# Optimization experiments

Hardware: AMD Instinct MI355X
Metric: run time of the kernel (lower is better)

Reference implementation:

```python
import math
import jax, jax.numpy as jnp
import numpy as np

D_MODEL, N_HEADS, D_FF = 2048, 16, 8192
B, T = 4, 1024
D_HEAD = D_MODEL // N_HEADS
LN_EPS = 1e-5


def hadamard(x):
    """Orthonormal Hadamard transform along last dim (power-of-two length)."""
    n = x.shape[-1]
    y = x.reshape(-1, n)
    h = 1
    while h < n:
        y = y.reshape(-1, n // (2 * h), 2, h)
        a, b = y[..., 0, :], y[..., 1, :]
        y = jnp.concatenate([a + b, a - b], axis=-1).reshape(-1, n)
        h *= 2
    return (y / math.sqrt(n)).reshape(x.shape)


def quantize_int8_per_row(W):
    s = jnp.maximum(jnp.max(jnp.abs(W), axis=1, keepdims=True), 1e-8) / 127.0
    Q = jnp.clip(jnp.round(W / s), -127, 127).astype(jnp.int8)
    return Q, s


def make_dtdr_weight(key, out_f, in_f):
    W = jax.random.normal(key, (out_f, in_f), dtype=jnp.float32) * 0.02
    return quantize_int8_per_row(hadamard(W))  # W_tilde = W @ H, then int8


def setup_inputs() -> dict:
    key = jax.random.key(0)
    ks = jax.random.split(key, 8)
    x = jax.random.normal(ks[0], (B, T, D_MODEL), dtype=jnp.float32)
    Qq, sq = make_dtdr_weight(ks[1], D_MODEL, D_MODEL)
    Qk, sk = make_dtdr_weight(ks[2], D_MODEL, D_MODEL)
    Qv, sv = make_dtdr_weight(ks[3], D_MODEL, D_MODEL)
    Qo, so = make_dtdr_weight(ks[4], D_MODEL, D_MODEL)
    Qf1, sf1 = make_dtdr_weight(ks[5], D_FF, D_MODEL)
    Qf2, sf2 = make_dtdr_weight(ks[6], D_MODEL, D_FF)
    return dict(
        x=x,
        ln1_g=jnp.ones((D_MODEL,), jnp.float32), ln1_b=jnp.zeros((D_MODEL,), jnp.float32),
        ln2_g=jnp.ones((D_MODEL,), jnp.float32), ln2_b=jnp.zeros((D_MODEL,), jnp.float32),
        Qq=Qq, sq=sq, Qk=Qk, sk=sk, Qv=Qv, sv=sv, Qo=Qo, so=so,
        Qf1=Qf1, sf1=sf1, bf1=jnp.zeros((D_FF,), jnp.float32),
        Qf2=Qf2, sf2=sf2, bf2=jnp.zeros((D_MODEL,), jnp.float32),
    )


def layernorm(x, g, b):
    mu = jnp.mean(x, axis=-1, keepdims=True)
    var = jnp.mean(jnp.square(x - mu), axis=-1, keepdims=True)
    return (x - mu) / jnp.sqrt(var + LN_EPS) * g + b


def dtdr_linear(x, Q, s, bias=None):
    # y = (H x) @ dequant(Q)^T + b
    xh = hadamard(x.astype(jnp.float32))
    W = Q.astype(jnp.float32) * s  # (out, in)
    y = jnp.einsum('btd,od->bto', xh, W)
    return y if bias is None else y + bias


def reference(x, ln1_g, ln1_b, ln2_g, ln2_b, Qq, sq, Qk, sk, Qv, sv, Qo, so,
              Qf1, sf1, bf1, Qf2, sf2, bf2):
    Bc, Tc, C = x.shape
    h = layernorm(x, ln1_g, ln1_b)
    q = dtdr_linear(h, Qq, sq).reshape(Bc, Tc, N_HEADS, D_HEAD).transpose(0, 2, 1, 3)
    k = dtdr_linear(h, Qk, sk).reshape(Bc, Tc, N_HEADS, D_HEAD).transpose(0, 2, 1, 3)
    v = dtdr_linear(h, Qv, sv).reshape(Bc, Tc, N_HEADS, D_HEAD).transpose(0, 2, 1, 3)
    scores = jnp.einsum('bhqd,bhkd->bhqk', q, k) / math.sqrt(D_HEAD)
    p = jax.nn.softmax(scores, axis=-1)
    out = jnp.einsum('bhqk,bhkd->bhqd', p, v)
    out = out.transpose(0, 2, 1, 3).reshape(Bc, Tc, C)
    x = x + dtdr_linear(out, Qo, so)
    h = layernorm(x, ln2_g, ln2_b)
    ff = dtdr_linear(h, Qf1, sf1, bf1)
    ff = jax.nn.gelu(ff, approximate=False)  # torch F.gelu default = erf gelu
    x = x + dtdr_linear(ff, Qf2, sf2, bf2)
    return x
```

## Files before the change

### kernel.cpp

```cpp
#include <hip/hip_runtime.h>
#include <cstdint>
#include <cstddef>

typedef unsigned short u16;
typedef unsigned int   u32;
typedef __bf16 bf16x8 __attribute__((ext_vector_type(8)));
typedef float  f32x4  __attribute__((ext_vector_type(4)));

__device__ __forceinline__ float bf2f(u16 u) {
  union { u32 i; float f; } v; v.i = ((u32)u) << 16; return v.f;
}
__device__ __forceinline__ u16 f2bf(float f) {
  union { float f; u32 i; } v; v.f = f;
  u32 r = v.i + 0x7fffu + ((v.i >> 16) & 1u);
  return (u16)(r >> 16);
}
__device__ __forceinline__ void unpack8(uint4 raw, float* v) {
  v[0]=bf2f(raw.x&0xffff); v[1]=bf2f(raw.x>>16);
  v[2]=bf2f(raw.y&0xffff); v[3]=bf2f(raw.y>>16);
  v[4]=bf2f(raw.z&0xffff); v[5]=bf2f(raw.z>>16);
  v[6]=bf2f(raw.w&0xffff); v[7]=bf2f(raw.w>>16);
}
__device__ __forceinline__ uint4 pack8(const float* v) {
  uint4 r;
  r.x = (u32)f2bf(v[0]) | ((u32)f2bf(v[1])<<16);
  r.y = (u32)f2bf(v[2]) | ((u32)f2bf(v[3])<<16);
  r.z = (u32)f2bf(v[4]) | ((u32)f2bf(v[5])<<16);
  r.w = (u32)f2bf(v[6]) | ((u32)f2bf(v[7])<<16);
  return r;
}
__device__ __forceinline__ void gload16(const void* g, void* l) {
  __builtin_amdgcn_global_load_lds((const __attribute__((address_space(1))) void*)g,
                                   (__attribute__((address_space(3))) void*)l, 16, 0, 0);
}
__device__ __forceinline__ int swz8(int row) { return ((row >> 3) ^ row) & 7; }

template<typename T>
__device__ __forceinline__ void load8(const T* p, float* v);
template<> __device__ __forceinline__ void load8<float>(const float* p, float* v) {
  const float4 a = ((const float4*)p)[0];
  const float4 b = ((const float4*)p)[1];
  v[0]=a.x; v[1]=a.y; v[2]=a.z; v[3]=a.w;
  v[4]=b.x; v[5]=b.y; v[6]=b.z; v[7]=b.w;
}
template<> __device__ __forceinline__ void load8<u16>(const u16* p, float* v) {
  unpack8(*(const uint4*)p, v);
}

__global__ __launch_bounds__(256) void cvt_k(const int* __restrict__ Q, u16* __restrict__ W) {
  const size_t i = ((size_t)blockIdx.x * 256 + threadIdx.x) * 8;
  const int4 a = *(const int4*)(Q + i);
  const int4 b = *(const int4*)(Q + i + 4);
  union { float f; u32 u; } c;
  uint4 r;
  u32 t;
  c.f = (float)a.x; t = c.u >> 16; c.f = (float)a.y; r.x = t | (c.u & 0xffff0000u);
  c.f = (float)a.z; t = c.u >> 16; c.f = (float)a.w; r.y = t | (c.u & 0xffff0000u);
  c.f = (float)b.x; t = c.u >> 16; c.f = (float)b.y; r.z = t | (c.u & 0xffff0000u);
  c.f = (float)b.z; t = c.u >> 16; c.f = (float)b.w; r.w = t | (c.u & 0xffff0000u);
  *(uint4*)(W + i) = r;
}

__global__ __launch_bounds__(256) void scat_k(const float* __restrict__ a,
    const float* __restrict__ b, const float* __restrict__ c, float* __restrict__ o) {
  const int i = blockIdx.x * 256 + threadIdx.x;
  o[i] = (i < 2048) ? a[i] : (i < 4096 ? b[i - 2048] : c[i - 4096]);
}

template<typename T>
__global__ __launch_bounds__(256) void ln_fwht_k(const T* __restrict__ X,
    const float* __restrict__ G, const float* __restrict__ Bt, u16* __restrict__ O) {
  __shared__ float buf[2048];
  __shared__ float red[8];
  const int tid = threadIdx.x;
  const int lane = tid & 63, wave = tid >> 6;
  const size_t base = (size_t)blockIdx.x * 2048;
  float v[8]; load8(X + base + tid*8, v);
  float s = 0.f, s2 = 0.f;
  for (int j = 0; j < 8; ++j) { s += v[j]; s2 += v[j]*v[j]; }
  for (int m = 1; m < 64; m <<= 1) { s += __shfl_xor(s, m, 64); s2 += __shfl_xor(s2, m, 64); }
  if (lane == 0) { red[wave] = s; red[4 + wave] = s2; }
  __syncthreads();
  s  = red[0] + red[1] + red[2] + red[3];
  s2 = red[4] + red[5] + red[6] + red[7];
  const float mu = s * (1.f/2048.f);
  const float rstd = rsqrtf(s2 * (1.f/2048.f) - mu*mu + 1e-5f);
  float g[8], bb[8];
  load8(G + tid*8, g); load8(Bt + tid*8, bb);
  for (int j = 0; j < 8; ++j) buf[tid*8 + j] = (v[j] - mu) * rstd * g[j] + bb[j];
  __syncthreads();
  for (int h = 1; h < 2048; h <<= 1) {
    for (int p = 0; p < 4; ++p) {
      const int idx = p*256 + tid;
      const int i = ((idx & ~(h-1)) << 1) | (idx & (h-1));
      const float a = buf[i], c = buf[i + h];
      buf[i] = a + c; buf[i + h] = a - c;
    }
    __syncthreads();
  }
  float o[8];
  for (int j = 0; j < 8; ++j) o[j] = buf[tid*8 + j] * 0.02209708691207961f;
  *(uint4*)&O[base + tid*8] = pack8(o);
}

template<int N>
__global__ __launch_bounds__(256) void fwht_ip(u16* __restrict__ D) {
  __shared__ float buf[N];
  const int tid = threadIdx.x;
  const size_t base = (size_t)blockIdx.x * N;
  constexpr int V8 = N / (8*256);
  for (int i = 0; i < V8; ++i) {
    uint4 raw = *(const uint4*)&D[base + (i*256 + tid)*8];
    float v[8]; unpack8(raw, v);
    for (int j = 0; j < 8; ++j) buf[(i*256 + tid)*8 + j] = v[j];
  }
  __syncthreads();
  constexpr int PAIRS = N / 2 / 256;
  for (int h = 1; h < N; h <<= 1) {
    for (int p = 0; p < PAIRS; ++p) {
      const int idx = p*256 + tid;
      const int i = ((idx & ~(h-1)) << 1) | (idx & (h-1));
      const float a = buf[i], c = buf[i + h];
      buf[i] = a + c; buf[i + h] = a - c;
    }
    __syncthreads();
  }
  const float sc = rsqrtf((float)N);
  for (int i = 0; i < V8; ++i) {
    float v[8];
    for (int j = 0; j < 8; ++j) v[j] = buf[(i*256 + tid)*8 + j] * sc;
    *(uint4*)&D[base + (i*256 + tid)*8] = pack8(v);
  }
}

__global__ __launch_bounds__(512, 1) void gemm256(
    const u16* __restrict__ A, const u16* __restrict__ Bw, const float* __restrict__ S,
    void* __restrict__ C, int ldc, int M, int N, int K,
    const float* __restrict__ bias, const float* __restrict__ resf,
    const u16* __restrict__ resb, int dogelu, int outf32)
{
  __shared__ alignas(16) u16 sA[3][256*64];
  __shared__ alignas(16) u16 sB[3][128*64];
  const int tid = threadIdx.x;
  const int lane = tid & 63, wave = tid >> 6;
  const int quad = lane >> 4, l16 = lane & 15;
  const int wm = wave & 3, wn = wave >> 2;
  const int nwg = gridDim.x * gridDim.y;
  int flat = blockIdx.y * gridDim.x + blockIdx.x;
  if ((nwg & 7) == 0) flat = (flat & 7) * (nwg >> 3) + (flat >> 3);
  const long tM = (long)(flat % gridDim.x) * 256;
  const long tN = (long)(flat / gridDim.x) * 128;

  const int rc = lane >> 3;
  const int cswz = ((lane & 7) ^ rc) * 8;
  const u16* Ab = A  + (size_t)(tM + rc) * K + cswz;
  const u16* Bb = Bw + (size_t)(tN + rc) * K + cswz;

  f32x4 acc[4][4] = {};
  const int ntk = K >> 6;

  auto stageA = [&](int buf, int k0, int i) {
    const int chunk = i*8 + wave;
    gload16(Ab + (size_t)(chunk*8)*K + k0, &sA[buf][chunk*512]);
  };
  auto stageB = [&](int buf, int k0, int i) {
    const int chunk = i*8 + wave;
    gload16(Bb + (size_t)(chunk*8)*K + k0, &sB[buf][chunk*512]);
  };

  stageA(0, 0, 0); stageA(0, 0, 1); stageA(0, 0, 2); stageA(0, 0, 3);
  stageB(0, 0, 0); stageB(0, 0, 1);
  if (ntk > 1) {
    stageA(1, 64, 0); stageA(1, 64, 1); stageA(1, 64, 2); stageA(1, 64, 3);
    stageB(1, 64, 0); stageB(1, 64, 1);
  }
  asm volatile("s_waitcnt vmcnt(6)" ::: "memory");
  __builtin_amdgcn_s_barrier();
  __builtin_amdgcn_sched_barrier(0);

  for (int t = 0; t < ntk; ++t) {
    const int buf = t % 3, nb = (t + 2) % 3;
    const bool more = (t + 2) < ntk;
    const int k2 = (t + 2) << 6;
    bf16x8 af[4], bq[4];
#pragma unroll
    for (int ks = 0; ks < 2; ++ks) {
      const int oc = ks*4 + quad;
#pragma unroll
      for (int mt = 0; mt < 4; ++mt)
        af[mt] = *(const bf16x8*)&sA[buf][(wm*64 + mt*16 + l16)*64 + (oc ^ (l16 & 7))*8];
#pragma unroll
      for (int nt = 0; nt < 4; ++nt)
        bq[nt] = *(const bf16x8*)&sB[buf][(wn*64 + nt*16 + l16)*64 + (oc ^ (l16 & 7))*8];
      if (more) {
        if (ks == 0) { stageA(nb, k2, 0); stageA(nb, k2, 1); stageB(nb, k2, 0); }
        else         { stageA(nb, k2, 2); stageA(nb, k2, 3); stageB(nb, k2, 1); }
      }
      if (ks == 1 && t + 1 < ntk) {
        if (more) asm volatile("s_waitcnt vmcnt(6)" ::: "memory");
        else      asm volatile("s_waitcnt vmcnt(0)" ::: "memory");
      }
      __builtin_amdgcn_s_barrier();
      __builtin_amdgcn_sched_barrier(0);
      __builtin_amdgcn_s_setprio(1);
#pragma unroll
      for (int mt = 0; mt < 4; ++mt)
#pragma unroll
        for (int nt = 0; nt < 4; ++nt)
          acc[mt][nt] = __builtin_amdgcn_mfma_f32_16x16x32_bf16(af[mt], bq[nt], acc[mt][nt], 0, 0, 0);
      __builtin_amdgcn_s_setprio(0);
      __builtin_amdgcn_s_barrier();
      __builtin_amdgcn_sched_barrier(0);
    }
  }

#pragma unroll
  for (int in = 0; in < 4; ++in) {
    const long col = tN + wn*64 + in*16 + l16;
    const float sc = S[col];
    const float bv = bias ? bias[col] : 0.f;
#pragma unroll
    for (int im = 0; im < 4; ++im) {
      const long row0 = tM + wm*64 + im*16 + quad*4;
#pragma unroll
      for (int r = 0; r < 4; ++r) {
        float v = acc[im][in][r] * sc + bv;
        if (dogelu) v = 0.5f * v * (1.f + erff(v * 0.7071067811865475f));
        const size_t off = (size_t)(row0 + r)*ldc + col;
        if (resf) v += resf[off];
        if (resb) v += bf2f(resb[off]);
        if (outf32) ((float*)C)[off] = v;
        else        ((u16*)C)[off]   = f2bf(v);
      }
    }
  }
}

__global__ __launch_bounds__(256, 2) void attn_k(const u16* __restrict__ QKV, u16* __restrict__ O)
{
  __shared__ alignas(16) u16 sKV[16384];
  __shared__ alignas(16) u16 sP[16384];
  const int tid = threadIdx.x;
  const int lane = tid & 63, wave = tid >> 6;
  const int quad = lane >> 4, l16 = lane & 15;
  const int qt = blockIdx.x;
  const int bh = blockIdx.y;
  const int b = bh >> 4, h = bh & 15;
  const size_t rb = (size_t)b * 1024;
  const u16* Qg = QKV + (rb + (size_t)qt*128)*6144 + h*128;
  const u16* Kg = QKV + rb*6144 + 2048 + h*128;
  const u16* Vg = QKV + rb*6144 + 4096 + h*128;

  for (int c = 0; c < 8; ++c) {
    const int chunk = c*4 + wave;
    const int r = chunk*4 + quad;
    gload16(Qg + (size_t)r*6144 + (l16 ^ swz8(r))*8, &sP[chunk*512]);
  }
  __syncthreads();
  bf16x8 aq[2][4];
  for (int im = 0; im < 2; ++im)
    for (int kk = 0; kk < 4; ++kk) {
      const int row = wave*32 + im*16 + l16;
      aq[im][kk] = *(const bf16x8*)&sP[row*128 + ((kk*4 + quad) ^ swz8(row))*8];
    }

  float mrun[2][4], lrun[2][4];
  f32x4 oacc[2][8] = {};
  for (int im = 0; im < 2; ++im)
    for (int r = 0; r < 4; ++r) { mrun[im][r] = -1e30f; lrun[im][r] = 0.f; }

  for (int kt = 0; kt < 8; ++kt) {
    __syncthreads();
    for (int c = 0; c < 8; ++c) {
      const int chunk = c*4 + wave;
      const int r = chunk*4 + quad;
      gload16(Kg + (size_t)(kt*128 + r)*6144 + (l16 ^ swz8(r))*8, &sKV[chunk*512]);
    }
    __syncthreads();
    f32x4 sf[2][8] = {};
#pragma unroll
    for (int kk = 0; kk < 4; ++kk)
#pragma unroll
      for (int jn = 0; jn < 8; ++jn) {
        const int rk = jn*16 + l16;
        const bf16x8 bk = *(const bf16x8*)&sKV[rk*128 + ((kk*4 + quad) ^ swz8(rk))*8];
        sf[0][jn] = __builtin_amdgcn_mfma_f32_16x16x32_bf16(aq[0][kk], bk, sf[0][jn], 0, 0, 0);
        sf[1][jn] = __builtin_amdgcn_mfma_f32_16x16x32_bf16(aq[1][kk], bk, sf[1][jn], 0, 0, 0);
      }
    const float scale = 0.08838834764831845f;
#pragma unroll
    for (int im = 0; im < 2; ++im)
#pragma unroll
      for (int r = 0; r < 4; ++r) {
        float mx = -1e30f;
        for (int jn = 0; jn < 8; ++jn) mx = fmaxf(mx, sf[im][jn][r] * scale);
        for (int m = 1; m < 16; m <<= 1) mx = fmaxf(mx, __shfl_xor(mx, m, 64));
        const float mold = mrun[im][r];
        const float mnew = fmaxf(mold, mx);
        const float alpha = __expf(mold - mnew);
        float ls = 0.f;
        const int rl = im*16 + quad*4 + r;
        for (int jn = 0; jn < 8; ++jn) {
          const float p = __expf(sf[im][jn][r] * scale - mnew);
          ls += p;
          sP[wave*4096 + rl*128 + (((jn*2 + (l16 >> 3)) ^ swz8(rl))*8 | (l16 & 7))] = f2bf(p);
        }
        for (int m = 1; m < 16; m <<= 1) ls += __shfl_xor(ls, m, 64);
        lrun[im][r] = lrun[im][r]*alpha + ls;
        mrun[im][r] = mnew;
        for (int od = 0; od < 8; ++od) oacc[im][od][r] *= alpha;
      }
    __syncthreads();
#pragma unroll
    for (int c = 0; c < 4; ++c) {
      const int task = c*256 + tid;
      const int kv = (task >> 4) * 2;
      const int d0 = (task & 15) * 8;
      const uint4 ra = *(const uint4*)(Vg + (size_t)(kt*128 + kv    )*6144 + d0);
      const uint4 rc = *(const uint4*)(Vg + (size_t)(kt*128 + kv + 1)*6144 + d0);
      const int cc = kv >> 3;
      const u16* pa = (const u16*)&ra;
      const u16* pb = (const u16*)&rc;
#pragma unroll
      for (int j = 0; j < 8; ++j) {
        const int row = d0 + j;
        const int col = ((cc ^ swz8(row))*8) | (kv & 7);
        *(u32*)&sKV[row*128 + col] = (u32)pa[j] | ((u32)pb[j] << 16);
      }
    }
    __syncthreads();
#pragma unroll
    for (int kk = 0; kk < 4; ++kk) {
      const int r0 = l16, r1 = 16 + l16;
      const bf16x8 ap0 = *(const bf16x8*)&sP[wave*4096 + r0*128 + ((kk*4 + quad) ^ swz8(r0))*8];
      const bf16x8 ap1 = *(const bf16x8*)&sP[wave*4096 + r1*128 + ((kk*4 + quad) ^ swz8(r1))*8];
#pragma unroll
      for (int od = 0; od < 8; ++od) {
        const int rv = od*16 + l16;
        const bf16x8 bv = *(const bf16x8*)&sKV[rv*128 + ((kk*4 + quad) ^ swz8(rv))*8];
        oacc[0][od] = __builtin_amdgcn_mfma_f32_16x16x32_bf16(ap0, bv, oacc[0][od], 0, 0, 0);
        oacc[1][od] = __builtin_amdgcn_mfma_f32_16x16x32_bf16(ap1, bv, oacc[1][od], 0, 0, 0);
      }
    }
  }
  for (int im = 0; im < 2; ++im)
    for (int r = 0; r < 4; ++r) {
      const float inv = 1.f / lrun[im][r];
      const size_t row = rb + (size_t)qt*128 + wave*32 + im*16 + quad*4 + r;
      for (int od = 0; od < 8; ++od)
        O[row*2048 + h*128 + od*16 + l16] = f2bf(oacc[im][od][r] * inv);
    }
}

extern "C" void kernel_launch(void* const* d_in, const int* in_sizes, int n_in,
                              void* d_out, int out_size, void* d_ws, size_t ws_size,
                              hipStream_t stream) {
  const float* x    = (const float*)d_in[0];
  const float* ln1g = (const float*)d_in[1];
  const float* ln1b = (const float*)d_in[2];
  const float* ln2g = (const float*)d_in[3];
  const float* ln2b = (const float*)d_in[4];
  const int* Qq  = (const int*)d_in[5];  const float* sq  = (const float*)d_in[6];
  const int* Qk  = (const int*)d_in[7];  const float* sk  = (const float*)d_in[8];
  const int* Qv  = (const int*)d_in[9];  const float* sv  = (const float*)d_in[10];
  const int* Qo  = (const int*)d_in[11]; const float* so  = (const float*)d_in[12];
  const int* Qf1 = (const int*)d_in[13]; const float* sf1 = (const float*)d_in[14];
  const float* bf1 = (const float*)d_in[15];
  const int* Qf2 = (const int*)d_in[16]; const float* sf2 = (const float*)d_in[17];
  const float* bf2 = (const float*)d_in[18];

  u16* XH   = (u16*)d_ws;
  u16* Wq   = XH + 8388608;
  u16* Wsl  = XH + 8388608;
  u16* QKVb = XH + 20971520;
  u16* FFb  = XH + 16777216;
  u16* Wf2  = XH;
  float* Scat = (float*)(XH + 46137344);
  float* Xout = (float*)d_out;
  if (ws_size < (size_t)100663296) return;

  ln_fwht_k<float><<<4096, 256, 0, stream>>>(x, ln1g, ln1b, XH);

  cvt_k<<<2048, 256, 0, stream>>>(Qq, Wq);
  cvt_k<<<2048, 256, 0, stream>>>(Qk, Wq + 4194304);
  cvt_k<<<2048, 256, 0, stream>>>(Qv, Wq + 8388608);
  scat_k<<<24, 256, 0, stream>>>(sq, sk, sv, Scat);
  gemm256<<<dim3(16,48), 512, 0, stream>>>(XH, Wq, Scat, QKVb, 6144, 4096, 6144, 2048,
                                           nullptr, nullptr, nullptr, 0, 0);

  attn_k<<<dim3(8, 64), 256, 0, stream>>>(QKVb, XH);

  fwht_ip<2048><<<4096, 256, 0, stream>>>(XH);

  cvt_k<<<2048, 256, 0, stream>>>(Qo, Wsl);
  gemm256<<<dim3(16,16), 512, 0, stream>>>(XH, Wsl, so, Xout, 2048, 4096, 2048, 2048,
                                           nullptr, x, nullptr, 0, 1);

  ln_fwht_k<float><<<4096, 256, 0, stream>>>(Xout, ln2g, ln2b, XH);

  cvt_k<<<4096, 256, 0, stream>>>(Qf1, Wsl);
  gemm256<<<dim3(16,32), 512, 0, stream>>>(XH, Wsl, sf1,        FFb + 0,    8192, 4096, 4096, 2048,
                                           bf1,        nullptr, nullptr, 1, 0);
  cvt_k<<<4096, 256, 0, stream>>>(Qf1 + (size_t)4096*2048, Wsl);
  gemm256<<<dim3(16,32), 512, 0, stream>>>(XH, Wsl, sf1 + 4096, FFb + 4096, 8192, 4096, 4096, 2048,
                                           bf1 + 4096, nullptr, nullptr, 1, 0);

  fwht_ip<8192><<<4096, 256, 0, stream>>>(FFb);

  cvt_k<<<8192, 256, 0, stream>>>(Qf2, Wf2);
  gemm256<<<dim3(16,16), 512, 0, stream>>>(FFb, Wf2, sf2, Xout, 2048, 4096, 2048, 8192,
                                           bf2, Xout, nullptr, 0, 1);
}
```

Before: 1.233 ms.

## Halve attention query tile to 64 rows and remap blocks across XCDs

The attention kernel now handles 64 query rows per workgroup instead of 128. The grid doubles to 1024 blocks, and the P buffer in shared memory and the register footprint shrink enough to allow 3 blocks per CU. A flat block-index remap groups blocks that share the same (batch, head) K/V onto the same XCD so they reuse data in L2. The trade-off is that each K/V tile is loaded and transposed twice as many times in total, and each wave issues fewer MFMAs per shared-memory read.

```diff
diff --git a/kernel.cpp b/kernel.cpp
--- a/kernel.cpp
+++ b/kernel.cpp
@@ -236,38 +236,41 @@
   }
 }
 
-__global__ __launch_bounds__(256, 2) void attn_k(const u16* __restrict__ QKV, u16* __restrict__ O)
+__global__ __launch_bounds__(256, 3) void attn_k(const u16* __restrict__ QKV, u16* __restrict__ O)
 {
   __shared__ alignas(16) u16 sKV[16384];
-  __shared__ alignas(16) u16 sP[16384];
+  __shared__ alignas(16) u16 sP[8192];
   const int tid = threadIdx.x;
   const int lane = tid & 63, wave = tid >> 6;
   const int quad = lane >> 4, l16 = lane & 15;
-  const int qt = blockIdx.x;
-  const int bh = blockIdx.y;
+  const int nwg = gridDim.x * gridDim.y;
+  int flat = blockIdx.y * gridDim.x + blockIdx.x;
+  flat = (flat & 7) * (nwg >> 3) + (flat >> 3);
+  const int qt = flat & 15;
+  const int bh = flat >> 4;
   const int b = bh >> 4, h = bh & 15;
   const size_t rb = (size_t)b * 1024;
-  const u16* Qg = QKV + (rb + (size_t)qt*128)*6144 + h*128;
+  const u16* Qg = QKV + (rb + (size_t)qt*64)*6144 + h*128;
   const u16* Kg = QKV + rb*6144 + 2048 + h*128;
   const u16* Vg = QKV + rb*6144 + 4096 + h*128;
 
-  for (int c = 0; c < 8; ++c) {
+  for (int c = 0; c < 4; ++c) {
     const int chunk = c*4 + wave;
     const int r = chunk*4 + quad;
     gload16(Qg + (size_t)r*6144 + (l16 ^ swz8(r))*8, &sP[chunk*512]);
   }
   __syncthreads();
-  bf16x8 aq[2][4];
-  for (int im = 0; im < 2; ++im)
-    for (int kk = 0; kk < 4; ++kk) {
-      const int row = wave*32 + im*16 + l16;
-      aq[im][kk] = *(const bf16x8*)&sP[row*128 + ((kk*4 + quad) ^ swz8(row))*8];
-    }
-
-  float mrun[2][4], lrun[2][4];
-  f32x4 oacc[2][8] = {};
-  for (int im = 0; im < 2; ++im)
-    for (int r = 0; r < 4; ++r) { mrun[im][r] = -1e30f; lrun[im][r] = 0.f; }
+  bf16x8 aq[4];
+#pragma unroll
+  for (int kk = 0; kk < 4; ++kk) {
+    const int row = wave*16 + l16;
+    aq[kk] = *(const bf16x8*)&sP[row*128 + ((kk*4 + quad) ^ swz8(row))*8];
+  }
+
+  float mrun[4], lrun[4];
+  f32x4 oacc[8] = {};
+#pragma unroll
+  for (int r = 0; r < 4; ++r) { mrun[r] = -1e30f; lrun[r] = 0.f; }
 
   for (int kt = 0; kt < 8; ++kt) {
     __syncthreads();
@@ -277,39 +280,36 @@
       gload16(Kg + (size_t)(kt*128 + r)*6144 + (l16 ^ swz8(r))*8, &sKV[chunk*512]);
     }
     __syncthreads();
-    f32x4 sf[2][8] = {};
+    f32x4 sf[8] = {};
 #pragma unroll
     for (int kk = 0; kk < 4; ++kk)
 #pragma unroll
       for (int jn = 0; jn < 8; ++jn) {
         const int rk = jn*16 + l16;
         const bf16x8 bk = *(const bf16x8*)&sKV[rk*128 + ((kk*4 + quad) ^ swz8(rk))*8];
-        sf[0][jn] = __builtin_amdgcn_mfma_f32_16x16x32_bf16(aq[0][kk], bk, sf[0][jn], 0, 0, 0);
-        sf[1][jn] = __builtin_amdgcn_mfma_f32_16x16x32_bf16(aq[1][kk], bk, sf[1][jn], 0, 0, 0);
+        sf[jn] = __builtin_amdgcn_mfma_f32_16x16x32_bf16(aq[kk], bk, sf[jn], 0, 0, 0);
       }
     const float scale = 0.08838834764831845f;
 #pragma unroll
-    for (int im = 0; im < 2; ++im)
-#pragma unroll
-      for (int r = 0; r < 4; ++r) {
-        float mx = -1e30f;
-        for (int jn = 0; jn < 8; ++jn) mx = fmaxf(mx, sf[im][jn][r] * scale);
-        for (int m = 1; m < 16; m <<= 1) mx = fmaxf(mx, __shfl_xor(mx, m, 64));
-        const float mold = mrun[im][r];
-        const float mnew = fmaxf(mold, mx);
-        const float alpha = __expf(mold - mnew);
-        float ls = 0.f;
-        const int rl = im*16 + quad*4 + r;
-        for (int jn = 0; jn < 8; ++jn) {
-          const float p = __expf(sf[im][jn][r] * scale - mnew);
-          ls += p;
-          sP[wave*4096 + rl*128 + (((jn*2 + (l16 >> 3)) ^ swz8(rl))*8 | (l16 & 7))] = f2bf(p);
-        }
-        for (int m = 1; m < 16; m <<= 1) ls += __shfl_xor(ls, m, 64);
-        lrun[im][r] = lrun[im][r]*alpha + ls;
-        mrun[im][r] = mnew;
-        for (int od = 0; od < 8; ++od) oacc[im][od][r] *= alpha;
-      }
+    for (int r = 0; r < 4; ++r) {
+      float mx = -1e30f;
+      for (int jn = 0; jn < 8; ++jn) mx = fmaxf(mx, sf[jn][r] * scale);
+      for (int m = 1; m < 16; m <<= 1) mx = fmaxf(mx, __shfl_xor(mx, m, 64));
+      const float mold = mrun[r];
+      const float mnew = fmaxf(mold, mx);
+      const float alpha = __expf(mold - mnew);
+      float ls = 0.f;
+      const int rl = quad*4 + r;
+      for (int jn = 0; jn < 8; ++jn) {
+        const float p = __expf(sf[jn][r] * scale - mnew);
+        ls += p;
+        sP[wave*2048 + rl*128 + (((jn*2 + (l16 >> 3)) ^ swz8(rl))*8 | (l16 & 7))] = f2bf(p);
+      }
+      for (int m = 1; m < 16; m <<= 1) ls += __shfl_xor(ls, m, 64);
+      lrun[r] = lrun[r]*alpha + ls;
+      mrun[r] = mnew;
+      for (int od = 0; od < 8; ++od) oacc[od][r] *= alpha;
+    }
     __syncthreads();
 #pragma unroll
     for (int c = 0; c < 4; ++c) {
@@ -317,10 +317,10 @@
       const int kv = (task >> 4) * 2;
       const int d0 = (task & 15) * 8;
       const uint4 ra = *(const uint4*)(Vg + (size_t)(kt*128 + kv    )*6144 + d0);
-      const uint4 rc = *(const uint4*)(Vg + (size_t)(kt*128 + kv + 1)*6144 + d0);
+      const uint4 rcx = *(const uint4*)(Vg + (size_t)(kt*128 + kv + 1)*6144 + d0);
       const int cc = kv >> 3;
       const u16* pa = (const u16*)&ra;
-      const u16* pb = (const u16*)&rc;
+      const u16* pb = (const u16*)&rcx;
 #pragma unroll
       for (int j = 0; j < 8; ++j) {
         const int row = d0 + j;
@@ -331,25 +331,22 @@
     __syncthreads();
 #pragma unroll
     for (int kk = 0; kk < 4; ++kk) {
-      const int r0 = l16, r1 = 16 + l16;
-      const bf16x8 ap0 = *(const bf16x8*)&sP[wave*4096 + r0*128 + ((kk*4 + quad) ^ swz8(r0))*8];
-      const bf16x8 ap1 = *(const bf16x8*)&sP[wave*4096 + r1*128 + ((kk*4 + quad) ^ swz8(r1))*8];
+      const bf16x8 ap = *(const bf16x8*)&sP[wave*2048 + l16*128 + ((kk*4 + quad) ^ swz8(l16))*8];
 #pragma unroll
       for (int od = 0; od < 8; ++od) {
         const int rv = od*16 + l16;
         const bf16x8 bv = *(const bf16x8*)&sKV[rv*128 + ((kk*4 + quad) ^ swz8(rv))*8];
-        oacc[0][od] = __builtin_amdgcn_mfma_f32_16x16x32_bf16(ap0, bv, oacc[0][od], 0, 0, 0);
-        oacc[1][od] = __builtin_amdgcn_mfma_f32_16x16x32_bf16(ap1, bv, oacc[1][od], 0, 0, 0);
-      }
-    }
-  }
-  for (int im = 0; im < 2; ++im)
-    for (int r = 0; r < 4; ++r) {
-      const float inv = 1.f / lrun[im][r];
-      const size_t row = rb + (size_t)qt*128 + wave*32 + im*16 + quad*4 + r;
-      for (int od = 0; od < 8; ++od)
-        O[row*2048 + h*128 + od*16 + l16] = f2bf(oacc[im][od][r] * inv);
-    }
+        oacc[od] = __builtin_amdgcn_mfma_f32_16x16x32_bf16(ap, bv, oacc[od], 0, 0, 0);
+      }
+    }
+  }
+#pragma unroll
+  for (int r = 0; r < 4; ++r) {
+    const float inv = 1.f / lrun[r];
+    const size_t row = rb + (size_t)qt*64 + wave*16 + quad*4 + r;
+    for (int od = 0; od < 8; ++od)
+      O[row*2048 + h*128 + od*16 + l16] = f2bf(oacc[od][r] * inv);
+  }
 }
 
 extern "C" void kernel_launch(void* const* d_in, const int* in_sizes, int n_in,
@@ -388,7 +385,7 @@
   gemm256<<<dim3(16,48), 512, 0, stream>>>(XH, Wq, Scat, QKVb, 6144, 4096, 6144, 2048,
                                            nullptr, nullptr, nullptr, 0, 0);
 
-  attn_k<<<dim3(8, 64), 256, 0, stream>>>(QKVb, XH);
+  attn_k<<<dim3(16, 64), 256, 0, stream>>>(QKVb, XH);
 
   fwht_ip<2048><<<4096, 256, 0, stream>>>(XH);
 
```

After: 1.226 ms. No clear change (-0.6%).
